# Kernel optimization log

Hardware: AMD Instinct MI355X
Metric: run time of the kernel (lower is better)

The kernel has to match this reference:

```python
import jax, jax.numpy as jnp
import numpy as np

B, L, D = 2, 2048, 1024
NUM_HEADS = 16
HEAD_DIM = D // NUM_HEADS


def setup_inputs() -> dict:
    key = jax.random.key(0)
    k1, k2 = jax.random.split(key)
    x = jax.random.normal(k1, (B, L, D), dtype=jnp.float32)
    # torch Linear(input_dim, 3*output_dim, bias=False); store as [in, 3*out] for x @ W
    W_qkv = jax.random.normal(k2, (D, 3 * D), dtype=jnp.float32) * (1.0 / np.sqrt(D))
    return {"x": x, "W_qkv": W_qkv}


def reference(x, W_qkv):
    b, l, d = x.shape
    h, hd = NUM_HEADS, HEAD_DIM
    qkv = x @ W_qkv                                  # [B, L, 3*D]
    qkv = qkv.reshape(b, l, 3, h, hd)
    q = jnp.transpose(qkv[:, :, 0], (0, 2, 1, 3))    # [B, H, L, hd]
    k = jnp.transpose(qkv[:, :, 1], (0, 2, 1, 3))
    v = jnp.transpose(qkv[:, :, 2], (0, 2, 1, 3))
    scale = 1.0 / jnp.sqrt(jnp.asarray(hd, dtype=x.dtype))
    scores = jnp.einsum('bhqd,bhkd->bhqk', q, k) * scale   # [B, H, L, L]
    causal = jnp.triu(jnp.ones((l, l), dtype=bool), k=1)   # True above diagonal -> masked
    scores = jnp.where(causal, -jnp.inf, scores)
    attn = jax.nn.softmax(scores, axis=-1)
    # dropout p=0.0 -> identity (eval mode)
    out = jnp.einsum('bhqk,bhkd->bhqd', attn, v)            # [B, H, L, hd]
    out = jnp.transpose(out, (0, 2, 1, 3)).reshape(b, l, h * hd)
    return out
```

## Files before the change

### kernel.cpp

```cpp
#include <hip/hip_runtime.h>
#include <hip/hip_bf16.h>
#include <math.h>

#define NB_L 2048
#define GM 4096
#define GN 3072
#define GK 1024
#define NROWS 65536
#define SCALE_L2E 0.180336880f

typedef float  f4v __attribute__((ext_vector_type(4)));
typedef short  s4v __attribute__((ext_vector_type(4)));
typedef short  s8v __attribute__((ext_vector_type(8)));

#define MFMA_16x16x32(a, b, c) __builtin_amdgcn_mfma_f32_16x16x32_bf16((a), (b), (c), 0, 0, 0)
#define MFMA_16x16x16(a, b, c) __builtin_amdgcn_mfma_f32_16x16x16bf16_1k((a), (b), (c), 0, 0, 0)

static __device__ __forceinline__ unsigned int bfpk(float a, float b) {
    __hip_bfloat162 h = __float22bfloat162_rn(float2{a, b});
    union { __hip_bfloat162 h2; unsigned int u; } cv; cv.h2 = h; return cv.u;
}
static __device__ __forceinline__ unsigned short bf1(float a) {
    union { __hip_bfloat16 h; unsigned short u; } cv; cv.h = __float2bfloat16(a); return cv.u;
}
static __device__ __forceinline__ float bf2f(unsigned short u) {
    union { unsigned int u; float f; } cv; cv.u = ((unsigned int)u) << 16; return cv.f;
}

static __device__ __forceinline__ void gl_lds16(const ushort* g, ushort* l) {
    __builtin_amdgcn_global_load_lds((const __attribute__((address_space(1))) void*)g,
                                     (__attribute__((address_space(3))) void*)l, 16, 0, 0);
}

__global__ __launch_bounds__(256) void conv_fused(
    const float* __restrict__ X, const float* __restrict__ W,
    ushort* __restrict__ Xb, ushort* __restrict__ Wt)
{
    __shared__ __align__(16) ushort T[64][72];
    const int bid = blockIdx.x, t = threadIdx.x;
    if (bid < 2048) {
        const int i = bid * 256 + t;
        const float4 f0 = ((const float4*)X)[2 * i];
        const float4 f1 = ((const float4*)X)[2 * i + 1];
        uint4 u;
        u.x = bfpk(f0.x, f0.y); u.y = bfpk(f0.z, f0.w);
        u.z = bfpk(f1.x, f1.y); u.w = bfpk(f1.z, f1.w);
        ((uint4*)Xb)[i] = u;
    } else {
        const int wb = bid - 2048;
        const int k0 = (wb & 15) * 64, n0 = (wb >> 4) * 64;
        {
            const int kr = t >> 2, nc0 = (t & 3) * 16;
            const float* src = W + (size_t)(k0 + kr) * GN + n0 + nc0;
#pragma unroll
            for (int u = 0; u < 4; ++u) {
                const float4 v = *(const float4*)(src + 4 * u);
                T[nc0 + 4 * u + 0][kr] = bf1(v.x);
                T[nc0 + 4 * u + 1][kr] = bf1(v.y);
                T[nc0 + 4 * u + 2][kr] = bf1(v.z);
                T[nc0 + 4 * u + 3][kr] = bf1(v.w);
            }
        }
        __syncthreads();
        {
            const int nr = t >> 2, kc0 = (t & 3) * 16;
            ushort* dst = Wt + (size_t)(n0 + nr) * GK + k0 + kc0;
            *(s8v*)dst       = *(const s8v*)&T[nr][kc0];
            *(s8v*)(dst + 8) = *(const s8v*)&T[nr][kc0 + 8];
        }
    }
}

__global__ __launch_bounds__(512, 2) void qkv_gemm_bf16(
    const ushort* __restrict__ Xb, const ushort* __restrict__ Wt,
    ushort* __restrict__ Qh, ushort* __restrict__ Kh, ushort* __restrict__ VT)
{
    __shared__ __align__(16) ushort As[2][2][128][32];
    __shared__ __align__(16) ushort Bs[2][2][384][32];

    const int tid = threadIdx.x;
    const int bid = blockIdx.x;

    const int xcd = bid & 7, idx = bid >> 3;
    const int ytile = ((xcd >> 1) << 3) + (idx & 7);
    const int xtile = ((xcd & 1) << 2) + (idx >> 3);
    const int row0 = ytile << 7;
    const int col0 = xtile * 384;

    const int lane = tid & 63, w = tid >> 6;
    const int wm = w >> 2, wn = w & 3;
    const int lq = lane & 15, quad = lane >> 4;

    const int rS = tid >> 2, pA = tid & 3;
    const int cA = pA ^ ((rS >> 1) & 3);
    const ushort* gA0 = Xb + (size_t)(row0 + rS) * GK + cA * 8;
    const ushort* gB0 = Wt + (size_t)(col0 + rS) * GK + cA * 8;

    const int pq = (quad ^ ((lq >> 1) & 3)) * 8;
    const int rowA = wm * 64 + lq;
    const int rowB = wn * 96 + lq;

    f4v acc[4][6];
#pragma unroll
    for (int mf = 0; mf < 4; ++mf)
#pragma unroll
        for (int nf = 0; nf < 6; ++nf) acc[mf][nf] = 0.f;

    auto stA = [&](int t, int h) {
        gl_lds16(gA0 + t * 64 + h * 32, &As[t & 1][h][rS][pA * 8]);
    };
    auto stB = [&](int t, int h, int u) {
        gl_lds16(gB0 + (size_t)u * 128 * GK + t * 64 + h * 32,
                 &Bs[t & 1][h][u * 128 + rS][pA * 8]);
    };

    stA(0, 0);
    stB(0, 0, 0); stB(0, 0, 1); stB(0, 0, 2);
    stA(0, 1);
    stB(0, 1, 0); stB(0, 1, 1); stB(0, 1, 2);
    stA(1, 0);
    stB(1, 0, 0); stB(1, 0, 1); stB(1, 0, 2);
    asm volatile("s_waitcnt vmcnt(4)" ::: "memory");
    __builtin_amdgcn_s_barrier();
    asm volatile("" ::: "memory");

    const int NT = GK / 64;
#pragma unroll 2
    for (int t = 0; t < NT; ++t) {
        const int cur = t & 1;
        s8v af[4], bfr[3];

#pragma unroll
        for (int nf = 0; nf < 3; ++nf) bfr[nf] = *(const s8v*)&Bs[cur][0][rowB + nf * 16][pq];
#pragma unroll
        for (int mf = 0; mf < 4; ++mf) af[mf] = *(const s8v*)&As[cur][0][rowA + mf * 16][pq];
        if (t + 1 < NT) { stB(t + 1, 1, 0); stB(t + 1, 1, 1); stB(t + 1, 1, 2); }
        __builtin_amdgcn_s_barrier();
        asm volatile("s_waitcnt lgkmcnt(0)");
        __builtin_amdgcn_s_setprio(1);
#pragma unroll
        for (int mf = 0; mf < 4; ++mf)
#pragma unroll
            for (int nf = 0; nf < 3; ++nf)
                acc[mf][nf] = MFMA_16x16x32(af[mf], bfr[nf], acc[mf][nf]);
        __builtin_amdgcn_s_setprio(0);
        __builtin_amdgcn_s_barrier();

#pragma unroll
        for (int nf = 0; nf < 3; ++nf) bfr[nf] = *(const s8v*)&Bs[cur][0][rowB + 48 + nf * 16][pq];
        if (t + 1 < NT) stA(t + 1, 1);
        __builtin_amdgcn_s_barrier();
        asm volatile("s_waitcnt lgkmcnt(0)");
        __builtin_amdgcn_s_setprio(1);
#pragma unroll
        for (int mf = 0; mf < 4; ++mf)
#pragma unroll
            for (int nf = 0; nf < 3; ++nf)
                acc[mf][nf + 3] = MFMA_16x16x32(af[mf], bfr[nf], acc[mf][nf + 3]);
        __builtin_amdgcn_s_setprio(0);
        __builtin_amdgcn_s_barrier();

#pragma unroll
        for (int nf = 0; nf < 3; ++nf) bfr[nf] = *(const s8v*)&Bs[cur][1][rowB + nf * 16][pq];
#pragma unroll
        for (int mf = 0; mf < 4; ++mf) af[mf] = *(const s8v*)&As[cur][1][rowA + mf * 16][pq];
        if (t + 2 < NT) stA(t + 2, 0);
        __builtin_amdgcn_s_barrier();
        asm volatile("s_waitcnt lgkmcnt(0)");
        __builtin_amdgcn_s_setprio(1);
#pragma unroll
        for (int mf = 0; mf < 4; ++mf)
#pragma unroll
            for (int nf = 0; nf < 3; ++nf)
                acc[mf][nf] = MFMA_16x16x32(af[mf], bfr[nf], acc[mf][nf]);
        __builtin_amdgcn_s_setprio(0);
        __builtin_amdgcn_s_barrier();

#pragma unroll
        for (int nf = 0; nf < 3; ++nf) bfr[nf] = *(const s8v*)&Bs[cur][1][rowB + 48 + nf * 16][pq];
        if (t + 2 < NT) { stB(t + 2, 0, 0); stB(t + 2, 0, 1); stB(t + 2, 0, 2); }
        __builtin_amdgcn_s_barrier();
        asm volatile("s_waitcnt lgkmcnt(0)");
        __builtin_amdgcn_s_setprio(1);
#pragma unroll
        for (int mf = 0; mf < 4; ++mf)
#pragma unroll
            for (int nf = 0; nf < 3; ++nf)
                acc[mf][nf + 3] = MFMA_16x16x32(af[mf], bfr[nf], acc[mf][nf + 3]);
        __builtin_amdgcn_s_setprio(0);
        if (t + 2 < NT) asm volatile("s_waitcnt vmcnt(4)" ::: "memory");
        else            asm volatile("s_waitcnt vmcnt(0)" ::: "memory");
        __builtin_amdgcn_s_barrier();
        asm volatile("" ::: "memory");
    }

#pragma unroll
    for (int mf = 0; mf < 4; ++mf)
#pragma unroll
        for (int nf = 0; nf < 6; ++nf) {
            const int colg = col0 + wn * 96 + nf * 16 + lq;
            const int part = colg >> 10;
            const int colp = colg & 1023;
            const int hh = colp >> 6, d = colp & 63;
#pragma unroll
            for (int r = 0; r < 4; ++r) {
                const int row = row0 + wm * 64 + mf * 16 + quad * 4 + r;
                const int b = row >> 11, tok = row & 2047;
                const int bh = b * 16 + hh;
                if (part == 0) {
                    Qh[((size_t)bh * 2048 + tok) * 64 + d] = bf1(acc[mf][nf][r] * SCALE_L2E);
                } else if (part == 1) {
                    Kh[((size_t)bh * 2048 + tok) * 64 + (d ^ ((tok & 7) << 3))] = bf1(acc[mf][nf][r]);
                } else {
                    VT[((size_t)bh * 64 + d) * 2048 + (tok ^ ((d & 7) << 3))] = bf1(acc[mf][nf][r]);
                }
            }
        }
}

__global__ __launch_bounds__(256, 4) void attn_bf16(
    const ushort* __restrict__ Qh, const ushort* __restrict__ Kh,
    const ushort* __restrict__ VT, ushort* __restrict__ Opart, float* __restrict__ Lp)
{
    __shared__ __align__(16) ushort Ks[2][64 * 64];
    __shared__ __align__(16) ushort Vt[2][64 * 64];

    const int x = blockIdx.x;
    const int bh = x & 31;
    const int y = x >> 5;
    const int s = y & 1;
    const int qp = y >> 1;

    const int tid = threadIdx.x;
    const int w = tid >> 6, lane = tid & 63;
    const int lq = lane & 15, quad = lane >> 4;
    const int kswz = (lq & 7) << 3;

    const ushort* kbase = Kh + (size_t)bh * 2048 * 64;
    const ushort* vbase = VT + (size_t)bh * 64 * 2048;
    const int g1 = tid, g2 = tid + 256;
    const int kr1 = g1 >> 3, ko1 = (g1 & 7) * 8;
    const int kr2 = g2 >> 3, ko2 = (g2 & 7) * 8;

    auto stage = [&](int kt, int bufi) {
        const ushort* kt_k = kbase + (size_t)kt * 64 * 64;
        const ushort* kt_v = vbase + kt * 64;
        gl_lds16(kt_k + kr1 * 64 + ko1,           &Ks[bufi][g1 * 8]);
        gl_lds16(kt_k + kr2 * 64 + ko2,           &Ks[bufi][g2 * 8]);
        gl_lds16(kt_v + (size_t)kr1 * 2048 + ko1, &Vt[bufi][g1 * 8]);
        gl_lds16(kt_v + (size_t)kr2 * 2048 + ko2, &Vt[bufi][g2 * 8]);
    };

    const s4v ones = { (short)0x3F80, (short)0x3F80, (short)0x3F80, (short)0x3F80 };

#pragma unroll 1
    for (int piece = 0; piece < 2; ++piece) {
        const int qt = piece ? (15 - qp) : qp;
        const int qrow_base = qt * 128 + w * 32;
        const int diag = 2 * qt + (w >> 1);
        const int kt_lo = s ? (qt + 1) : 0;
        const int niter = qt + 1;

        if (piece) __builtin_amdgcn_s_barrier();

        s8v qf[2][2];
#pragma unroll
        for (int qg = 0; qg < 2; ++qg)
#pragma unroll
            for (int sb = 0; sb < 2; ++sb)
                qf[qg][sb] = *(const s8v*)(Qh + ((size_t)bh * 2048 + qrow_base + qg * 16 + lq) * 64
                                           + sb * 32 + quad * 8);

        f4v o[4][2];
#pragma unroll
        for (int dg = 0; dg < 4; ++dg)
#pragma unroll
            for (int qg = 0; qg < 2; ++qg) o[dg][qg] = 0.f;
        f4v lacc[2]; lacc[0] = 0.f; lacc[1] = 0.f;

        auto compute = [&](int ktc, int bufi) {
            if (ktc > diag) return;
            f4v st[4][2];
#pragma unroll
            for (int kg = 0; kg < 4; ++kg)
#pragma unroll
                for (int qg = 0; qg < 2; ++qg) st[kg][qg] = 0.f;
#pragma unroll
            for (int kg = 0; kg < 4; ++kg)
#pragma unroll
                for (int sb = 0; sb < 2; ++sb) {
                    const s8v af = *(const s8v*)&Ks[bufi][(kg * 16 + lq) * 64
                                                         + ((sb * 32 + quad * 8) ^ kswz)];
#pragma unroll
                    for (int qg = 0; qg < 2; ++qg)
                        st[kg][qg] = MFMA_16x16x32(af, qf[qg][sb], st[kg][qg]);
                }
            if (ktc == diag) {
#pragma unroll
                for (int kg = 0; kg < 4; ++kg)
#pragma unroll
                    for (int qg = 0; qg < 2; ++qg) {
                        const int qrow = qrow_base + qg * 16 + lq;
#pragma unroll
                        for (int r = 0; r < 4; ++r)
                            if (ktc * 64 + kg * 16 + quad * 4 + r > qrow)
                                st[kg][qg][r] = -INFINITY;
                    }
            }
#pragma unroll
            for (int kg = 0; kg < 4; ++kg)
#pragma unroll
                for (int qg = 0; qg < 2; ++qg)
#pragma unroll
                    for (int r = 0; r < 4; ++r)
                        st[kg][qg][r] = exp2f(st[kg][qg][r]);
#pragma unroll
            for (int ks = 0; ks < 4; ++ks) {
                s4v pb[2];
#pragma unroll
                for (int qg = 0; qg < 2; ++qg) {
                    union { s4v v; uint2 u; } c;
                    c.u.x = bfpk(st[ks][qg][0], st[ks][qg][1]);
                    c.u.y = bfpk(st[ks][qg][2], st[ks][qg][3]);
                    pb[qg] = c.v;
                }
#pragma unroll
                for (int qg = 0; qg < 2; ++qg)
                    lacc[qg] = MFMA_16x16x16(ones, pb[qg], lacc[qg]);
#pragma unroll
                for (int dg = 0; dg < 4; ++dg) {
                    const s4v va = *(const s4v*)&Vt[bufi][(dg * 16 + lq) * 64
                                                         + ((ks * 16 + quad * 4) ^ kswz)];
#pragma unroll
                    for (int qg = 0; qg < 2; ++qg)
                        o[dg][qg] = MFMA_16x16x16(va, pb[qg], o[dg][qg]);
                }
            }
        };

        stage(kt_lo, 0);
#pragma unroll 1
        for (int i = 0; i < niter; ++i) {
            const int cur = i & 1;
            __builtin_amdgcn_s_barrier();
            if (i + 1 < niter) {
                stage(kt_lo + i + 1, cur ^ 1);
                asm volatile("s_waitcnt vmcnt(4)" ::: "memory");
            } else {
                asm volatile("s_waitcnt vmcnt(0)" ::: "memory");
            }
            __builtin_amdgcn_s_barrier();
            compute(kt_lo + i, cur);
        }

#pragma unroll
        for (int qg = 0; qg < 2; ++qg) {
            const size_t prow = (size_t)(s * 32 + bh) * 2048 + qrow_base + qg * 16 + lq;
#pragma unroll
            for (int dg = 0; dg < 4; ++dg) {
                const int d = dg * 16 + quad * 4;
                uint2 u;
                u.x = bfpk(o[dg][qg][0], o[dg][qg][1]);
                u.y = bfpk(o[dg][qg][2], o[dg][qg][3]);
                *(uint2*)&Opart[prow * 64 + d] = u;
            }
            if (quad == 0) Lp[prow] = lacc[qg][0];
        }
    }
}

__global__ __launch_bounds__(256) void attn_combine(
    const ushort* __restrict__ Opart, const float* __restrict__ Lp, float* __restrict__ Out)
{
    const int id = blockIdx.x * 256 + threadIdx.x;
    const int row = id >> 4, c4 = (id & 15) * 4;
    const float l0 = Lp[row], l1 = Lp[row + NROWS];
    const float inv = 1.0f / (l0 + l1);

    const s4v a = *(const s4v*)&Opart[(size_t)row * 64 + c4];
    const s4v c = *(const s4v*)&Opart[(size_t)(row + NROWS) * 64 + c4];
    float4 v;
    v.x = (bf2f((unsigned short)a[0]) + bf2f((unsigned short)c[0])) * inv;
    v.y = (bf2f((unsigned short)a[1]) + bf2f((unsigned short)c[1])) * inv;
    v.z = (bf2f((unsigned short)a[2]) + bf2f((unsigned short)c[2])) * inv;
    v.w = (bf2f((unsigned short)a[3]) + bf2f((unsigned short)c[3])) * inv;

    const int bh = row >> 11, qrow = row & 2047;
    const int b = bh >> 4, h = bh & 15;
    *(float4*)(Out + ((size_t)(b * 2048 + qrow)) * 1024 + h * 64 + c4) = v;
}

extern "C" void kernel_launch(void* const* d_in, const int* in_sizes, int n_in,
                              void* d_out, int out_size, void* d_ws, size_t ws_size,
                              hipStream_t stream)
{
    const float* x  = (const float*)d_in[0];
    const float* wq = (const float*)d_in[1];
    float* out = (float*)d_out;

    const size_t HEADTEN = (size_t)32 * 2048 * 64;
    ushort* wsp = (ushort*)d_ws;
    ushort* qh = wsp;
    ushort* kh = qh + HEADTEN;
    ushort* vt = kh + HEADTEN;
    ushort* xb = vt + HEADTEN;
    ushort* wt = xb + (size_t)GM * GK;
    ushort* opart = xb;
    float*  lp    = (float*)(opart + (size_t)2 * NROWS * 64);

    conv_fused<<<2816, 256, 0, stream>>>(x, wq, xb, wt);
    qkv_gemm_bf16<<<256, 512, 0, stream>>>(xb, wt, qh, kh, vt);
    attn_bf16<<<512, 256, 0, stream>>>(qh, kh, vt, opart, lp);
    attn_combine<<<NROWS * 16 / 256, 256, 0, stream>>>(opart, lp, out);
}
```

Measured before the change: 173.3 us.

## Restructure QKV GEMM main loop into 4-stage 32-wide K pipeline

```diff
diff --git a/kernel.cpp b/kernel.cpp
--- a/kernel.cpp
+++ b/kernel.cpp
@@ -75,8 +75,8 @@
     const ushort* __restrict__ Xb, const ushort* __restrict__ Wt,
     ushort* __restrict__ Qh, ushort* __restrict__ Kh, ushort* __restrict__ VT)
 {
-    __shared__ __align__(16) ushort As[2][2][128][32];
-    __shared__ __align__(16) ushort Bs[2][2][384][32];
+    __shared__ __align__(16) ushort As[4][128][32];
+    __shared__ __align__(16) ushort Bs[4][384][32];
 
     const int tid = threadIdx.x;
     const int bid = blockIdx.x;
@@ -106,92 +106,40 @@
 #pragma unroll
         for (int nf = 0; nf < 6; ++nf) acc[mf][nf] = 0.f;
 
-    auto stA = [&](int t, int h) {
-        gl_lds16(gA0 + t * 64 + h * 32, &As[t & 1][h][rS][pA * 8]);
+    auto stage = [&](int t) {
+        const int bi = t & 3;
+        gl_lds16(gA0 + t * 32, &As[bi][rS][pA * 8]);
+        gl_lds16(gB0 + t * 32,                          &Bs[bi][rS][pA * 8]);
+        gl_lds16(gB0 + (size_t)128 * GK + t * 32,       &Bs[bi][128 + rS][pA * 8]);
+        gl_lds16(gB0 + (size_t)256 * GK + t * 32,       &Bs[bi][256 + rS][pA * 8]);
     };
-    auto stB = [&](int t, int h, int u) {
-        gl_lds16(gB0 + (size_t)u * 128 * GK + t * 64 + h * 32,
-                 &Bs[t & 1][h][u * 128 + rS][pA * 8]);
-    };
-
-    stA(0, 0);
-    stB(0, 0, 0); stB(0, 0, 1); stB(0, 0, 2);
-    stA(0, 1);
-    stB(0, 1, 0); stB(0, 1, 1); stB(0, 1, 2);
-    stA(1, 0);
-    stB(1, 0, 0); stB(1, 0, 1); stB(1, 0, 2);
-    asm volatile("s_waitcnt vmcnt(4)" ::: "memory");
-    __builtin_amdgcn_s_barrier();
-    asm volatile("" ::: "memory");
-
-    const int NT = GK / 64;
-#pragma unroll 2
+
+    stage(0); stage(1); stage(2);
+
+    const int NT = GK / 32;
+#pragma unroll 4
     for (int t = 0; t < NT; ++t) {
-        const int cur = t & 1;
-        s8v af[4], bfr[3];
-
-#pragma unroll
-        for (int nf = 0; nf < 3; ++nf) bfr[nf] = *(const s8v*)&Bs[cur][0][rowB + nf * 16][pq];
-#pragma unroll
-        for (int mf = 0; mf < 4; ++mf) af[mf] = *(const s8v*)&As[cur][0][rowA + mf * 16][pq];
-        if (t + 1 < NT) { stB(t + 1, 1, 0); stB(t + 1, 1, 1); stB(t + 1, 1, 2); }
+        if (t + 2 < NT)      asm volatile("s_waitcnt vmcnt(8)" ::: "memory");
+        else if (t + 1 < NT) asm volatile("s_waitcnt vmcnt(4)" ::: "memory");
+        else                 asm volatile("s_waitcnt vmcnt(0)" ::: "memory");
         __builtin_amdgcn_s_barrier();
+
+        if (t + 3 < NT) stage(t + 3);
+
+        const int bi = t & 3;
+        s8v af[4], bfr[6];
+#pragma unroll
+        for (int mf = 0; mf < 4; ++mf) af[mf]  = *(const s8v*)&As[bi][rowA + mf * 16][pq];
+#pragma unroll
+        for (int nf = 0; nf < 6; ++nf) bfr[nf] = *(const s8v*)&Bs[bi][rowB + nf * 16][pq];
         asm volatile("s_waitcnt lgkmcnt(0)");
         __builtin_amdgcn_s_setprio(1);
 #pragma unroll
         for (int mf = 0; mf < 4; ++mf)
 #pragma unroll
-            for (int nf = 0; nf < 3; ++nf)
+            for (int nf = 0; nf < 6; ++nf)
                 acc[mf][nf] = MFMA_16x16x32(af[mf], bfr[nf], acc[mf][nf]);
         __builtin_amdgcn_s_setprio(0);
-        __builtin_amdgcn_s_barrier();
-
-#pragma unroll
-        for (int nf = 0; nf < 3; ++nf) bfr[nf] = *(const s8v*)&Bs[cur][0][rowB + 48 + nf * 16][pq];
-        if (t + 1 < NT) stA(t + 1, 1);
-        __builtin_amdgcn_s_barrier();
-        asm volatile("s_waitcnt lgkmcnt(0)");
-        __builtin_amdgcn_s_setprio(1);
-#pragma unroll
-        for (int mf = 0; mf < 4; ++mf)
-#pragma unroll
-            for (int nf = 0; nf < 3; ++nf)
-                acc[mf][nf + 3] = MFMA_16x16x32(af[mf], bfr[nf], acc[mf][nf + 3]);
-        __builtin_amdgcn_s_setprio(0);
-        __builtin_amdgcn_s_barrier();
-
-#pragma unroll
-        for (int nf = 0; nf < 3; ++nf) bfr[nf] = *(const s8v*)&Bs[cur][1][rowB + nf * 16][pq];
-#pragma unroll
-        for (int mf = 0; mf < 4; ++mf) af[mf] = *(const s8v*)&As[cur][1][rowA + mf * 16][pq];
-        if (t + 2 < NT) stA(t + 2, 0);
-        __builtin_amdgcn_s_barrier();
-        asm volatile("s_waitcnt lgkmcnt(0)");
-        __builtin_amdgcn_s_setprio(1);
-#pragma unroll
-        for (int mf = 0; mf < 4; ++mf)
-#pragma unroll
-            for (int nf = 0; nf < 3; ++nf)
-                acc[mf][nf] = MFMA_16x16x32(af[mf], bfr[nf], acc[mf][nf]);
-        __builtin_amdgcn_s_setprio(0);
-        __builtin_amdgcn_s_barrier();
-
-#pragma unroll
-        for (int nf = 0; nf < 3; ++nf) bfr[nf] = *(const s8v*)&Bs[cur][1][rowB + 48 + nf * 16][pq];
-        if (t + 2 < NT) { stB(t + 2, 0, 0); stB(t + 2, 0, 1); stB(t + 2, 0, 2); }
-        __builtin_amdgcn_s_barrier();
-        asm volatile("s_waitcnt lgkmcnt(0)");
-        __builtin_amdgcn_s_setprio(1);
-#pragma unroll
-        for (int mf = 0; mf < 4; ++mf)
-#pragma unroll
-            for (int nf = 0; nf < 3; ++nf)
-                acc[mf][nf + 3] = MFMA_16x16x32(af[mf], bfr[nf], acc[mf][nf + 3]);
-        __builtin_amdgcn_s_setprio(0);
-        if (t + 2 < NT) asm volatile("s_waitcnt vmcnt(4)" ::: "memory");
-        else            asm volatile("s_waitcnt vmcnt(0)" ::: "memory");
-        __builtin_amdgcn_s_barrier();
-        asm volatile("" ::: "memory");
     }
 
 #pragma unroll
```

Result: slower. 179.4 us (+3.5%).
